# Optimization experiments

Measured on AMD Instinct MI355X. Metric: run time of the kernel, lower is better.

Reference implementation:

```python
import jax, jax.numpy as jnp
import numpy as np

N, E, B = 100000, 3200000, 512
D_IN, D_H, HID = 500, 64, 200
NUM_CLASSES = 80
EPS_BN = 1e-5


def _sage(x, src, dst, Wl, bl, Wr):
    # PyG SAGEConv (mean aggr): out = lin_l(mean_{j->i} x_j) + lin_r(x_i)
    n = x.shape[0]
    agg = jax.ops.segment_sum(x[src], dst, num_segments=n)          # [n, d_in]
    deg = jax.ops.segment_sum(jnp.ones((src.shape[0],), x.dtype), dst, num_segments=n)
    mean = agg / jnp.maximum(deg, 1.0)[:, None]
    return mean @ Wl + bl + x @ Wr


def _bn(c, g, b):
    # BatchNorm1d, training-mode batch statistics (biased var)
    mu = c.mean(0)
    var = c.var(0)
    return (c - mu) / jnp.sqrt(var + EPS_BN) * g + b


def setup_inputs() -> dict:
    key = jax.random.key(0)
    ks = jax.random.split(key, 16)
    p = lambda k, shape: jax.random.normal(k, shape, dtype=jnp.float32) * 0.05
    z = lambda d: jnp.zeros((d,), jnp.float32)
    o = lambda d: jnp.ones((d,), jnp.float32)
    return {
        "x": jax.random.uniform(ks[0], (N, D_IN), dtype=jnp.float32),
        "edge_index": jax.random.randint(ks[1], (2, E), 0, N),
        "batch": jnp.sort(jax.random.randint(ks[2], (N,), 0, B)),
        "y": jax.random.randint(ks[3], (B,), 0, NUM_CLASSES),
        "conv1_Wl": p(ks[4], (D_IN, D_H)), "conv1_bl": z(D_H), "conv1_Wr": p(ks[5], (D_IN, D_H)),
        "conv2_Wl": p(ks[6], (D_H, D_H)),  "conv2_bl": z(D_H), "conv2_Wr": p(ks[7], (D_H, D_H)),
        "conv3_Wl": p(ks[8], (D_H, D_H)),  "conv3_bl": z(D_H), "conv3_Wr": p(ks[9], (D_H, D_H)),
        "lin1_W": p(ks[10], (D_H, HID)), "lin1_b": z(HID),
        "bn1_g": o(HID), "bn1_beta": z(HID),
        "lin2_W": p(ks[11], (HID, HID // 2)), "lin2_b": z(HID // 2),
        "bn2_g": o(HID // 2), "bn2_beta": z(HID // 2),
        "lin3_W": p(ks[12], (HID // 2, HID // 2)), "lin3_b": z(HID // 2),
        "bn3_g": o(HID // 2), "bn3_beta": z(HID // 2),
        "lin4_W": p(ks[13], (HID // 2, NUM_CLASSES)), "lin4_b": z(NUM_CLASSES),
    }


def reference(x, edge_index, batch, y,
              conv1_Wl, conv1_bl, conv1_Wr,
              conv2_Wl, conv2_bl, conv2_Wr,
              conv3_Wl, conv3_bl, conv3_Wr,
              lin1_W, lin1_b, bn1_g, bn1_beta,
              lin2_W, lin2_b, bn2_g, bn2_beta,
              lin3_W, lin3_b, bn3_g, bn3_beta,
              lin4_W, lin4_b):
    src, dst = edge_index[0], edge_index[1]
    # F.normalize(x, p=1.0, dim=-1)
    xn = x / jnp.maximum(jnp.abs(x).sum(-1, keepdims=True), 1e-12)
    e = _sage(xn, src, dst, conv1_Wl, conv1_bl, conv1_Wr)
    e = _sage(e, src, dst, conv2_Wl, conv2_bl, conv2_Wr)
    e = _sage(e, src, dst, conv3_Wl, conv3_bl, conv3_Wr)
    # global_mean_pool over graph ids
    sums = jax.ops.segment_sum(e, batch, num_segments=B)             # [B, 64]
    cnts = jax.ops.segment_sum(jnp.ones((e.shape[0],), e.dtype), batch, num_segments=B)
    c = sums / jnp.maximum(cnts, 1.0)[:, None]
    # dropout (p=0.1) omitted for a deterministic reference
    c = c @ lin1_W + lin1_b
    b = jnp.tanh(_bn(c, bn1_g, bn1_beta))
    c = b @ lin2_W + lin2_b
    b = jnp.tanh(_bn(c, bn2_g, bn2_beta))
    c = b @ lin3_W + lin3_b
    b = jnp.tanh(_bn(c, bn3_g, bn3_beta))
    return b @ lin4_W + lin4_b                                       # [B, 80]
```

## Files before the change

### kernel.cpp

```cpp
#include <hip/hip_runtime.h>
#include <hip/hip_bf16.h>

#define NN 100000
#define NE 3200000
#define NB 512
#define DIN 500
#define DH 64
#define HIDN 200
#define NCLS 80

#define NBUK 256
#define NPB 391
#define EPB 16384
#define NBLK_E ((NE + EPB - 1) / EPB)

typedef __attribute__((ext_vector_type(8))) short bf16x8;
typedef __attribute__((ext_vector_type(4))) float f32x4;

__device__ __forceinline__ short f2bf(float f) {
    union { float f; unsigned u; } v; v.f = f;
    unsigned r = v.u + 0x7FFF + ((v.u >> 16) & 1);
    return (short)(r >> 16);
}
__device__ __forceinline__ float bf2f(short s) {
    union { unsigned u; float f; } v; v.u = ((unsigned)(unsigned short)s) << 16;
    return v.f;
}

__global__ void bukhist_kernel(const int* __restrict__ dst, int* __restrict__ block_hist) {
    __shared__ int h[NBUK];
    for (int i = threadIdx.x; i < NBUK; i += 256) h[i] = 0;
    __syncthreads();
    int base = blockIdx.x * EPB;
    int end = min(base + EPB, NE);
    for (int e = base + threadIdx.x; e < end; e += 256)
        atomicAdd(&h[dst[e] / NPB], 1);
    __syncthreads();
    for (int i = threadIdx.x; i < NBUK; i += 256)
        block_hist[blockIdx.x * NBUK + i] = h[i];
}

__global__ void bukoff_kernel(int* __restrict__ block_hist, int* __restrict__ buk_base) {
    __shared__ int tot[NBUK];
    __shared__ int sc[NBUK];
    int b = threadIdx.x;
    int s = 0;
    for (int i = 0; i < NBLK_E; ++i) s += block_hist[i * NBUK + b];
    tot[b] = s; sc[b] = s;
    __syncthreads();
    for (int o = 1; o < NBUK; o <<= 1) {
        int t = (b >= o) ? sc[b - o] : 0;
        __syncthreads();
        sc[b] += t;
        __syncthreads();
    }
    int excl = sc[b] - tot[b];
    buk_base[b] = excl;
    if (b == NBUK - 1) buk_base[NBUK] = excl + tot[b];
    int run = excl;
    for (int i = 0; i < NBLK_E; ++i) {
        int idx = i * NBUK + b;
        int v = block_hist[idx];
        block_hist[idx] = run;
        run += v;
    }
}

__global__ void bukscat_kernel(const int* __restrict__ src, const int* __restrict__ dst,
                               const int* __restrict__ block_hist, int* __restrict__ bpack) {
    __shared__ int cur[NBUK];
    for (int i = threadIdx.x; i < NBUK; i += 256)
        cur[i] = block_hist[blockIdx.x * NBUK + i];
    __syncthreads();
    int base = blockIdx.x * EPB;
    int end = min(base + EPB, NE);
    for (int e = base + threadIdx.x; e < end; e += 256) {
        int d = dst[e];
        int bk = d / NPB;
        int p = atomicAdd(&cur[bk], 1);
        bpack[p] = (src[e] << 9) | (d - bk * NPB);
    }
}

__global__ void bukfin_kernel(const int* __restrict__ buk_base, const int* __restrict__ bpack,
                              int* __restrict__ row_ptr, float* __restrict__ invdeg,
                              int* __restrict__ csr_src) {
    __shared__ int cnt[NPB];
    __shared__ int cbase[NPB];
    int bk = blockIdx.x;
    int n0 = bk * NPB;
    int nloc = min(n0 + NPB, NN) - n0;
    for (int i = threadIdx.x; i < nloc; i += 256) cnt[i] = 0;
    __syncthreads();
    int beg = buk_base[bk], end = buk_base[bk + 1];
    for (int p = beg + threadIdx.x; p < end; p += 256)
        atomicAdd(&cnt[bpack[p] & 511], 1);
    __syncthreads();
    if (threadIdx.x == 0) {
        int run = beg;
        for (int i = 0; i < nloc; ++i) { int v = cnt[i]; cbase[i] = run; run += v; }
    }
    __syncthreads();
    for (int i = threadIdx.x; i < nloc; i += 256) {
        row_ptr[n0 + i] = cbase[i];
        invdeg[n0 + i] = 1.0f / fmaxf((float)cnt[i], 1.0f);
        cnt[i] = cbase[i];
    }
    if (bk == NBUK - 1 && threadIdx.x == 0) row_ptr[NN] = end;
    __syncthreads();
    for (int p = beg + threadIdx.x; p < end; p += 256) {
        int v = bpack[p];
        int q = atomicAdd(&cnt[v & 511], 1);
        csr_src[q] = v >> 9;
    }
}

__global__ void wprep_kernel(const float* __restrict__ Wl, const float* __restrict__ Wr,
                             short* __restrict__ Wb, int K, int KP) {
    int id = blockIdx.x * blockDim.x + threadIdx.x;
    if (id >= 128 * KP) return;
    int col = id / KP, k = id - col * KP;
    float v = 0.f;
    if (k < K) v = (col < 64) ? Wl[(size_t)k * 64 + col] : Wr[(size_t)k * 64 + (col - 64)];
    Wb[(size_t)col * KP + k] = f2bf(v);
}

template<int KP, int KREAL, bool SCALE>
__launch_bounds__(256)
__global__ void gemm_mfma_pipe(const float* __restrict__ in, const short* __restrict__ Wb,
                               short* __restrict__ Hl, short* __restrict__ Hr) {
    __shared__ short A_lds[2][64][40];
    __shared__ short B_lds[2][128][40];
    __shared__ float s_red[64][4];
    const int tid = threadIdx.x;
    const int row0 = blockIdx.x * 64;
    const int w = tid >> 6, l = tid & 63;
    const int q = l >> 4, r16 = l & 15;
    const int sa_row = tid >> 2;
    const int sa_kc  = (tid & 3) * 8;
    const int ga_row = row0 + sa_row;
    const bool row_ok = ga_row < NN;
    const float* arow = in + (size_t)ga_row * KREAL;
    const int sb_col = tid >> 1;
    const int sb_kh  = (tid & 1) * 16;
    const short* bsrc = Wb + (size_t)sb_col * KP + sb_kh;

    f32x4 acc[8];
#pragma unroll
    for (int c = 0; c < 8; ++c) acc[c] = (f32x4){0.f, 0.f, 0.f, 0.f};
    float pabs = 0.f;
    float va[8];
    bf16x8 vb0, vb1;
    constexpr int NT = KP / 32;

    auto loadA = [&](int t) {
        int gk = t * 32 + sa_kc;
#pragma unroll
        for (int i = 0; i < 8; i += 4) {
            if (row_ok && (KP == KREAL || gk + i + 3 < KREAL)) {
                const float4 f = *(const float4*)(arow + gk + i);
                va[i] = f.x; va[i + 1] = f.y; va[i + 2] = f.z; va[i + 3] = f.w;
            } else {
#pragma unroll
                for (int j = 0; j < 4; ++j)
                    va[i + j] = (row_ok && gk + i + j < KREAL) ? arow[gk + i + j] : 0.f;
            }
        }
    };
    auto loadB = [&](int t) {
        vb0 = *(const bf16x8*)(bsrc + t * 32);
        vb1 = *(const bf16x8*)(bsrc + t * 32 + 8);
    };
    auto store = [&](int buf) {
        short s[8];
#pragma unroll
        for (int i = 0; i < 8; ++i) {
            if (SCALE) pabs += fabsf(va[i]);
            s[i] = f2bf(va[i]);
        }
        *(bf16x8*)&A_lds[buf][sa_row][sa_kc] = *(bf16x8*)s;
        *(bf16x8*)&B_lds[buf][sb_col][sb_kh] = vb0;
        *(bf16x8*)&B_lds[buf][sb_col][sb_kh + 8] = vb1;
    };

    loadA(0); loadB(0);
    store(0);
    __syncthreads();
    int cur = 0;
    for (int t = 0; t < NT; ++t) {
        if (t + 1 < NT) { loadA(t + 1); loadB(t + 1); }
        bf16x8 a = *(bf16x8*)&A_lds[cur][w * 16 + r16][q * 8];
#pragma unroll
        for (int c = 0; c < 8; ++c) {
            bf16x8 b = *(bf16x8*)&B_lds[cur][c * 16 + r16][q * 8];
            acc[c] = __builtin_amdgcn_mfma_f32_16x16x32_bf16(a, b, acc[c], 0, 0, 0);
        }
        if (t + 1 < NT) {
            store(cur ^ 1);
            __syncthreads();
            cur ^= 1;
        }
    }

    if (SCALE) {
        __syncthreads();
        s_red[sa_row][tid & 3] = pabs;
        __syncthreads();
        if (tid < 64) {
            float ss = s_red[tid][0] + s_red[tid][1] + s_red[tid][2] + s_red[tid][3];
            s_red[tid][0] = 1.0f / fmaxf(ss, 1e-12f);
        }
        __syncthreads();
    }

#pragma unroll
    for (int c = 0; c < 8; ++c) {
#pragma unroll
        for (int rr = 0; rr < 4; ++rr) {
            int lrow = w * 16 + q * 4 + rr;
            int grow = row0 + lrow;
            if (grow < NN) {
                float o = acc[c][rr];
                if (SCALE) o *= s_red[lrow][0];
                short ob = f2bf(o);
                if (c < 4) Hl[(size_t)grow * 64 + c * 16 + r16] = ob;
                else       Hr[(size_t)grow * 64 + (c - 4) * 16 + r16] = ob;
            }
        }
    }
}

__launch_bounds__(256)
__global__ void gemm64_mfma(const short* __restrict__ ein, const short* __restrict__ Wb,
                            short* __restrict__ Hl, short* __restrict__ Hr) {
    const int tid = threadIdx.x;
    const int row0 = blockIdx.x * 64;
    const int w = tid >> 6, l = tid & 63;
    const int q = l >> 4, r16 = l & 15;
    const int arow = row0 + w * 16 + r16;
    const bool ok = arow < NN;
    const short* ap = ein + (size_t)(ok ? arow : 0) * 64 + q * 8;
    f32x4 acc[8];
#pragma unroll
    for (int c = 0; c < 8; ++c) acc[c] = (f32x4){0.f, 0.f, 0.f, 0.f};
    const bf16x8 z8 = (bf16x8){0, 0, 0, 0, 0, 0, 0, 0};
#pragma unroll
    for (int t = 0; t < 2; ++t) {
        bf16x8 a = ok ? *(const bf16x8*)(ap + t * 32) : z8;
#pragma unroll
        for (int c = 0; c < 8; ++c) {
            bf16x8 b = *(const bf16x8*)(Wb + (size_t)(c * 16 + r16) * 64 + t * 32 + q * 8);
            acc[c] = __builtin_amdgcn_mfma_f32_16x16x32_bf16(a, b, acc[c], 0, 0, 0);
        }
    }
#pragma unroll
    for (int c = 0; c < 8; ++c) {
#pragma unroll
        for (int rr = 0; rr < 4; ++rr) {
            int grow = row0 + w * 16 + q * 4 + rr;
            if (grow < NN) {
                short ob = f2bf(acc[c][rr]);
                if (c < 4) Hl[(size_t)grow * 64 + c * 16 + r16] = ob;
                else       Hr[(size_t)grow * 64 + (c - 4) * 16 + r16] = ob;
            }
        }
    }
}

__launch_bounds__(256)
__global__ void gather_kernel(const int* __restrict__ row_ptr, const int* __restrict__ csr_src,
                              const short* __restrict__ Hl, const short* __restrict__ Hr,
                              const float* __restrict__ invdeg, const float* __restrict__ bl,
                              short* __restrict__ eout) {
    int node = blockIdx.x * 4 + (threadIdx.x >> 6);
    if (node >= NN) return;
    int lane = threadIdx.x & 63;
    int ng = lane >> 3;
    int fl = lane & 7;
    int beg = row_ptr[node], end = row_ptr[node + 1];
    float a0[8], a1[8];
#pragma unroll
    for (int j = 0; j < 8; ++j) { a0[j] = 0.f; a1[j] = 0.f; }
    int p = beg + ng;
    for (; p + 8 < end; p += 16) {
        int s0 = csr_src[p];
        int s1 = csr_src[p + 8];
        bf16x8 v0 = *(const bf16x8*)(Hl + (size_t)s0 * 64 + fl * 8);
        bf16x8 v1 = *(const bf16x8*)(Hl + (size_t)s1 * 64 + fl * 8);
#pragma unroll
        for (int j = 0; j < 8; ++j) { a0[j] += bf2f(v0[j]); a1[j] += bf2f(v1[j]); }
    }
    if (p < end) {
        int s0 = csr_src[p];
        bf16x8 v0 = *(const bf16x8*)(Hl + (size_t)s0 * 64 + fl * 8);
#pragma unroll
        for (int j = 0; j < 8; ++j) a0[j] += bf2f(v0[j]);
    }
#pragma unroll
    for (int j = 0; j < 8; ++j) a0[j] += a1[j];
#pragma unroll
    for (int m = 8; m < 64; m <<= 1)
#pragma unroll
        for (int j = 0; j < 8; ++j) a0[j] += __shfl_xor(a0[j], m, 64);
    if (ng == 0) {
        float idg = invdeg[node];
        bf16x8 hr = *(const bf16x8*)(Hr + (size_t)node * 64 + fl * 8);
        short o[8];
#pragma unroll
        for (int j = 0; j < 8; ++j)
            o[j] = f2bf(a0[j] * idg + bl[fl * 8 + j] + bf2f(hr[j]));
        *(bf16x8*)(eout + (size_t)node * 64 + fl * 8) = *(bf16x8*)o;
    }
}

__global__ void gseg_kernel(const int* __restrict__ batch, int* __restrict__ gstart) {
    int i = blockIdx.x * blockDim.x + threadIdx.x;
    if (i >= NN) return;
    int bc = batch[i];
    int bp = (i == 0) ? -1 : batch[i - 1];
    for (int b = bp + 1; b <= bc; ++b) gstart[b] = i;
    if (i == NN - 1)
        for (int b = bc + 1; b <= NB; ++b) gstart[b] = NN;
}

__launch_bounds__(256)
__global__ void pool_seg(const short* __restrict__ e, const int* __restrict__ gstart,
                         float* __restrict__ c0) {
    __shared__ float part[4][64];
    int b = blockIdx.x;
    int w = threadIdx.x >> 6, lane = threadIdx.x & 63;
    int s = gstart[b], t = gstart[b + 1];
    float acc = 0.f;
    for (int i = s + w; i < t; i += 4) acc += bf2f(e[(size_t)i * 64 + lane]);
    part[w][lane] = acc;
    __syncthreads();
    if (w == 0) {
        float v = part[0][lane] + part[1][lane] + part[2][lane] + part[3][lane];
        c0[b * 64 + lane] = v / fmaxf((float)(t - s), 1.0f);
    }
}

__global__ void lin_kernel(const float* __restrict__ in, const float* __restrict__ W,
                           const float* __restrict__ bias, float* __restrict__ out,
                           int Kd, int Dout) {
    int id = blockIdx.x * blockDim.x + threadIdx.x;
    if (id >= NB * Dout) return;
    int row = id / Dout, col = id - row * Dout;
    const float* ir = in + (size_t)row * Kd;
    float acc = bias[col];
    for (int k = 0; k < Kd; ++k) acc += ir[k] * W[(size_t)k * Dout + col];
    out[id] = acc;
}

__global__ void bnstats_kernel(const float* __restrict__ c, const float* __restrict__ g,
                               const float* __restrict__ beta, float* __restrict__ sa,
                               float* __restrict__ sb, int Dout) {
    int col = blockIdx.x;
    int tid = threadIdx.x;
    float s = 0.f, sq = 0.f;
    for (int r = tid; r < NB; r += 256) {
        float v = c[(size_t)r * Dout + col];
        s += v; sq += v * v;
    }
    __shared__ float ls[256], lq[256];
    ls[tid] = s; lq[tid] = sq;
    __syncthreads();
    for (int o = 128; o > 0; o >>= 1) {
        if (tid < o) { ls[tid] += ls[tid + o]; lq[tid] += lq[tid + o]; }
        __syncthreads();
    }
    if (tid == 0) {
        float mu = ls[0] / NB;
        float var = lq[0] / NB - mu * mu;
        float a = g[col] * rsqrtf(var + 1e-5f);
        sa[col] = a;
        sb[col] = beta[col] - mu * a;
    }
}

__global__ void bnapply_kernel(const float* __restrict__ c, const float* __restrict__ sa,
                               const float* __restrict__ sb, float* __restrict__ bv, int Dout) {
    int id = blockIdx.x * blockDim.x + threadIdx.x;
    if (id >= NB * Dout) return;
    int col = id % Dout;
    bv[id] = tanhf(c[id] * sa[col] + sb[col]);
}

extern "C" void kernel_launch(void* const* d_in, const int* in_sizes, int n_in,
                              void* d_out, int out_size, void* d_ws, size_t ws_size,
                              hipStream_t stream) {
    const float* x    = (const float*)d_in[0];
    const int* ei     = (const int*)d_in[1];
    const int* src    = ei;
    const int* dst    = ei + NE;
    const int* batch  = (const int*)d_in[2];
    const float* c1Wl = (const float*)d_in[4];
    const float* c1bl = (const float*)d_in[5];
    const float* c1Wr = (const float*)d_in[6];
    const float* c2Wl = (const float*)d_in[7];
    const float* c2bl = (const float*)d_in[8];
    const float* c2Wr = (const float*)d_in[9];
    const float* c3Wl = (const float*)d_in[10];
    const float* c3bl = (const float*)d_in[11];
    const float* c3Wr = (const float*)d_in[12];
    const float* l1W  = (const float*)d_in[13]; const float* l1b = (const float*)d_in[14];
    const float* bn1g = (const float*)d_in[15]; const float* bn1b = (const float*)d_in[16];
    const float* l2W  = (const float*)d_in[17]; const float* l2b = (const float*)d_in[18];
    const float* bn2g = (const float*)d_in[19]; const float* bn2b = (const float*)d_in[20];
    const float* l3W  = (const float*)d_in[21]; const float* l3b = (const float*)d_in[22];
    const float* bn3g = (const float*)d_in[23]; const float* bn3b = (const float*)d_in[24];
    const float* l4W  = (const float*)d_in[25]; const float* l4b = (const float*)d_in[26];
    float* out = (float*)d_out;

    char* wsb = (char*)d_ws;
    short* Hl     = (short*)wsb; wsb += (size_t)NN * 64 * 2;
    short* Hr     = (short*)wsb; wsb += (size_t)NN * 64 * 2;
    short* e      = (short*)wsb; wsb += (size_t)NN * 64 * 2;
    float* invdeg = (float*)wsb; wsb += (size_t)NN * 4;
    float* c      = (float*)wsb; wsb += (size_t)NB * HIDN * 4;
    float* bv     = (float*)wsb; wsb += (size_t)NB * HIDN * 4;
    float* sa     = (float*)wsb; wsb += HIDN * 4;
    float* sb     = (float*)wsb; wsb += HIDN * 4;
    short* Wb1    = (short*)wsb; wsb += 128 * 512 * 2;
    short* Wb2    = (short*)wsb; wsb += 128 * 64 * 2;
    short* Wb3    = (short*)wsb; wsb += 128 * 64 * 2;
    int* row_ptr  = (int*)wsb;   wsb += (size_t)(NN + 1) * 4;
    int* csr_src  = (int*)wsb;   wsb += (size_t)NE * 4;
    int* buk_base = (int*)wsb;   wsb += (NBUK + 1) * 4;
    int* gstart   = (int*)wsb;   wsb += (NB + 1) * 4;
    int* bpack      = (int*)Hl;
    int* block_hist = (int*)e;

    bukhist_kernel<<<NBLK_E, 256, 0, stream>>>(dst, block_hist);
    bukoff_kernel<<<1, NBUK, 0, stream>>>(block_hist, buk_base);
    bukscat_kernel<<<NBLK_E, 256, 0, stream>>>(src, dst, block_hist, bpack);
    bukfin_kernel<<<NBUK, 256, 0, stream>>>(buk_base, bpack, row_ptr, invdeg, csr_src);

    gseg_kernel<<<(NN + 255) / 256, 256, 0, stream>>>(batch, gstart);

    wprep_kernel<<<(128 * 512 + 255) / 256, 256, 0, stream>>>(c1Wl, c1Wr, Wb1, DIN, 512);
    wprep_kernel<<<(128 * 64 + 255) / 256, 256, 0, stream>>>(c2Wl, c2Wr, Wb2, DH, 64);
    wprep_kernel<<<(128 * 64 + 255) / 256, 256, 0, stream>>>(c3Wl, c3Wr, Wb3, DH, 64);

    const int GB = (NN + 63) / 64;
    const int GGB = (NN + 3) / 4;

    gemm_mfma_pipe<512, DIN, true><<<GB, 256, 0, stream>>>(x, Wb1, Hl, Hr);
    gather_kernel<<<GGB, 256, 0, stream>>>(row_ptr, csr_src, Hl, Hr, invdeg, c1bl, e);
    gemm64_mfma<<<GB, 256, 0, stream>>>(e, Wb2, Hl, Hr);
    gather_kernel<<<GGB, 256, 0, stream>>>(row_ptr, csr_src, Hl, Hr, invdeg, c2bl, e);
    gemm64_mfma<<<GB, 256, 0, stream>>>(e, Wb3, Hl, Hr);
    gather_kernel<<<GGB, 256, 0, stream>>>(row_ptr, csr_src, Hl, Hr, invdeg, c3bl, e);

    pool_seg<<<NB, 256, 0, stream>>>(e, gstart, bv);

    lin_kernel<<<(NB * 200 + 255) / 256, 256, 0, stream>>>(bv, l1W, l1b, c, 64, 200);
    bnstats_kernel<<<200, 256, 0, stream>>>(c, bn1g, bn1b, sa, sb, 200);
    bnapply_kernel<<<(NB * 200 + 255) / 256, 256, 0, stream>>>(c, sa, sb, bv, 200);

    lin_kernel<<<(NB * 100 + 255) / 256, 256, 0, stream>>>(bv, l2W, l2b, c, 200, 100);
    bnstats_kernel<<<100, 256, 0, stream>>>(c, bn2g, bn2b, sa, sb, 100);
    bnapply_kernel<<<(NB * 100 + 255) / 256, 256, 0, stream>>>(c, sa, sb, bv, 100);

    lin_kernel<<<(NB * 100 + 255) / 256, 256, 0, stream>>>(bv, l3W, l3b, c, 100, 100);
    bnstats_kernel<<<100, 256, 0, stream>>>(c, bn3g, bn3b, sa, sb, 100);
    bnapply_kernel<<<(NB * 100 + 255) / 256, 256, 0, stream>>>(c, sa, sb, bv, 100);

    lin_kernel<<<(NB * 80 + 255) / 256, 256, 0, stream>>>(bv, l4W, l4b, out, 100, 80);
}
```

Before: 575.8 us.

## Enlarge first GEMM tile, keep Hr and final embeddings in fp32, deepen gather unroll

The first SAGE GEMM now processes 128 rows per block, with each wave computing two 16-row fragments that share the B loads, and uses a two-stage register prefetch over the 500-wide input. The root-term Hr and the last layer's output are now stored in fp32 instead of bf16, which adds memory traffic but improves accuracy. The gather loop is unrolled to four outstanding neighbour loads per lane, and its launch bounds request 8 blocks per CU. Together these aim to cut per-tile overhead in the large GEMM and to hide gather latency, at the cost of more registers and more bytes moved for Hr.

Result: slower. 608.4 us (+5.7%).

```diff
diff --git a/kernel.cpp b/kernel.cpp
--- a/kernel.cpp
+++ b/kernel.cpp
@@ -125,114 +125,112 @@
     Wb[(size_t)col * KP + k] = f2bf(v);
 }
 
-template<int KP, int KREAL, bool SCALE>
 __launch_bounds__(256)
 __global__ void gemm_mfma_pipe(const float* __restrict__ in, const short* __restrict__ Wb,
-                               short* __restrict__ Hl, short* __restrict__ Hr) {
-    __shared__ short A_lds[2][64][40];
+                               short* __restrict__ Hl, float* __restrict__ Hr) {
+    __shared__ short A_lds[2][128][40];
     __shared__ short B_lds[2][128][40];
-    __shared__ float s_red[64][4];
+    __shared__ float s_red[128][2];
     const int tid = threadIdx.x;
-    const int row0 = blockIdx.x * 64;
+    const int row0 = blockIdx.x * 128;
     const int w = tid >> 6, l = tid & 63;
     const int q = l >> 4, r16 = l & 15;
-    const int sa_row = tid >> 2;
-    const int sa_kc  = (tid & 3) * 8;
+    const int sa_row = tid >> 1;
+    const int sa_kc  = (tid & 1) * 16;
     const int ga_row = row0 + sa_row;
     const bool row_ok = ga_row < NN;
-    const float* arow = in + (size_t)ga_row * KREAL;
-    const int sb_col = tid >> 1;
-    const int sb_kh  = (tid & 1) * 16;
-    const short* bsrc = Wb + (size_t)sb_col * KP + sb_kh;
-
-    f32x4 acc[8];
-#pragma unroll
-    for (int c = 0; c < 8; ++c) acc[c] = (f32x4){0.f, 0.f, 0.f, 0.f};
+    const float* arow = in + (size_t)ga_row * DIN + sa_kc;
+    const short* bsrc = Wb + (size_t)sa_row * 512 + sa_kc;
+
+    f32x4 acc0[8], acc1[8];
+#pragma unroll
+    for (int c = 0; c < 8; ++c) { acc0[c] = (f32x4){0.f,0.f,0.f,0.f}; acc1[c] = (f32x4){0.f,0.f,0.f,0.f}; }
     float pabs = 0.f;
-    float va[8];
-    bf16x8 vb0, vb1;
-    constexpr int NT = KP / 32;
-
-    auto loadA = [&](int t) {
-        int gk = t * 32 + sa_kc;
-#pragma unroll
-        for (int i = 0; i < 8; i += 4) {
-            if (row_ok && (KP == KREAL || gk + i + 3 < KREAL)) {
-                const float4 f = *(const float4*)(arow + gk + i);
-                va[i] = f.x; va[i + 1] = f.y; va[i + 2] = f.z; va[i + 3] = f.w;
-            } else {
-#pragma unroll
-                for (int j = 0; j < 4; ++j)
-                    va[i + j] = (row_ok && gk + i + j < KREAL) ? arow[gk + i + j] : 0.f;
-            }
-        }
-    };
-    auto loadB = [&](int t) {
-        vb0 = *(const bf16x8*)(bsrc + t * 32);
-        vb1 = *(const bf16x8*)(bsrc + t * 32 + 8);
-    };
-    auto store = [&](int buf) {
-        short s[8];
-#pragma unroll
-        for (int i = 0; i < 8; ++i) {
-            if (SCALE) pabs += fabsf(va[i]);
-            s[i] = f2bf(va[i]);
-        }
-        *(bf16x8*)&A_lds[buf][sa_row][sa_kc] = *(bf16x8*)s;
-        *(bf16x8*)&B_lds[buf][sb_col][sb_kh] = vb0;
-        *(bf16x8*)&B_lds[buf][sb_col][sb_kh + 8] = vb1;
-    };
-
-    loadA(0); loadB(0);
-    store(0);
-    __syncthreads();
-    int cur = 0;
-    for (int t = 0; t < NT; ++t) {
-        if (t + 1 < NT) { loadA(t + 1); loadB(t + 1); }
-        bf16x8 a = *(bf16x8*)&A_lds[cur][w * 16 + r16][q * 8];
-#pragma unroll
-        for (int c = 0; c < 8; ++c) {
-            bf16x8 b = *(bf16x8*)&B_lds[cur][c * 16 + r16][q * 8];
-            acc[c] = __builtin_amdgcn_mfma_f32_16x16x32_bf16(a, b, acc[c], 0, 0, 0);
-        }
-        if (t + 1 < NT) {
-            store(cur ^ 1);
-            __syncthreads();
-            cur ^= 1;
-        }
-    }
-
-    if (SCALE) {
+    float va0[16], va1[16];
+    bf16x8 vb00, vb01, vb10, vb11;
+
+#define ISSUE(T, S) do { \
+    _Pragma("unroll") \
+    for (int i = 0; i < 16; i += 4) { \
+        int gk = (T) * 32 + sa_kc + i; \
+        float4 f = (row_ok && gk < DIN) ? *(const float4*)(arow + (T) * 32 + i) \
+                                        : make_float4(0.f, 0.f, 0.f, 0.f); \
+        va##S[i] = f.x; va##S[i+1] = f.y; va##S[i+2] = f.z; va##S[i+3] = f.w; \
+    } \
+    vb##S##0 = *(const bf16x8*)(bsrc + (T) * 32); \
+    vb##S##1 = *(const bf16x8*)(bsrc + (T) * 32 + 8); \
+} while (0)
+
+#define STAGE(BUF, S) do { \
+    short sh[16]; \
+    _Pragma("unroll") \
+    for (int i = 0; i < 16; ++i) { pabs += fabsf(va##S[i]); sh[i] = f2bf(va##S[i]); } \
+    *(bf16x8*)&A_lds[BUF][sa_row][sa_kc]     = *(bf16x8*)&sh[0]; \
+    *(bf16x8*)&A_lds[BUF][sa_row][sa_kc + 8] = *(bf16x8*)&sh[8]; \
+    *(bf16x8*)&B_lds[BUF][sa_row][sa_kc]     = vb##S##0; \
+    *(bf16x8*)&B_lds[BUF][sa_row][sa_kc + 8] = vb##S##1; \
+} while (0)
+
+#define COMPUTE(BUF) do { \
+    bf16x8 a0 = *(bf16x8*)&A_lds[BUF][w * 32 + r16][q * 8]; \
+    bf16x8 a1 = *(bf16x8*)&A_lds[BUF][w * 32 + 16 + r16][q * 8]; \
+    _Pragma("unroll") \
+    for (int c = 0; c < 8; ++c) { \
+        bf16x8 b = *(bf16x8*)&B_lds[BUF][c * 16 + r16][q * 8]; \
+        acc0[c] = __builtin_amdgcn_mfma_f32_16x16x32_bf16(a0, b, acc0[c], 0, 0, 0); \
+        acc1[c] = __builtin_amdgcn_mfma_f32_16x16x32_bf16(a1, b, acc1[c], 0, 0, 0); \
+    } \
+} while (0)
+
+    ISSUE(0, 0); ISSUE(1, 1);
+    STAGE(0, 0);
+    __syncthreads();
+    for (int tt = 0; tt < 8; ++tt) {
+        int t0 = tt * 2;
+        if (tt < 7) ISSUE(t0 + 2, 0);
+        COMPUTE(0);
+        STAGE(1, 1);
         __syncthreads();
-        s_red[sa_row][tid & 3] = pabs;
-        __syncthreads();
-        if (tid < 64) {
-            float ss = s_red[tid][0] + s_red[tid][1] + s_red[tid][2] + s_red[tid][3];
-            s_red[tid][0] = 1.0f / fmaxf(ss, 1e-12f);
-        }
-        __syncthreads();
-    }
-
-#pragma unroll
-    for (int c = 0; c < 8; ++c) {
-#pragma unroll
-        for (int rr = 0; rr < 4; ++rr) {
-            int lrow = w * 16 + q * 4 + rr;
-            int grow = row0 + lrow;
-            if (grow < NN) {
-                float o = acc[c][rr];
-                if (SCALE) o *= s_red[lrow][0];
-                short ob = f2bf(o);
-                if (c < 4) Hl[(size_t)grow * 64 + c * 16 + r16] = ob;
-                else       Hr[(size_t)grow * 64 + (c - 4) * 16 + r16] = ob;
-            }
-        }
-    }
+        if (tt < 7) ISSUE(t0 + 3, 1);
+        COMPUTE(1);
+        if (tt < 7) { STAGE(0, 0); __syncthreads(); }
+    }
+#undef ISSUE
+#undef STAGE
+#undef COMPUTE
+
+    __syncthreads();
+    s_red[sa_row][tid & 1] = pabs;
+    __syncthreads();
+    if (tid < 128) {
+        float ss = s_red[tid][0] + s_red[tid][1];
+        s_red[tid][0] = 1.0f / fmaxf(ss, 1e-12f);
+    }
+    __syncthreads();
+
+#define EPI(RF, ACC) do { \
+    _Pragma("unroll") \
+    for (int c = 0; c < 8; ++c) { \
+        _Pragma("unroll") \
+        for (int rr = 0; rr < 4; ++rr) { \
+            int lrow = w * 32 + (RF) * 16 + q * 4 + rr; \
+            int grow = row0 + lrow; \
+            if (grow < NN) { \
+                float o = ACC[c][rr] * s_red[lrow][0]; \
+                if (c < 4) Hl[(size_t)grow * 64 + c * 16 + r16] = f2bf(o); \
+                else       Hr[(size_t)grow * 64 + (c - 4) * 16 + r16] = o; \
+            } \
+        } \
+    } \
+} while (0)
+    EPI(0, acc0);
+    EPI(1, acc1);
+#undef EPI
 }
 
 __launch_bounds__(256)
 __global__ void gemm64_mfma(const short* __restrict__ ein, const short* __restrict__ Wb,
-                            short* __restrict__ Hl, short* __restrict__ Hr) {
+                            short* __restrict__ Hl, float* __restrict__ Hr) {
     const int tid = threadIdx.x;
     const int row0 = blockIdx.x * 64;
     const int w = tid >> 6, l = tid & 63;
@@ -259,19 +257,19 @@
         for (int rr = 0; rr < 4; ++rr) {
             int grow = row0 + w * 16 + q * 4 + rr;
             if (grow < NN) {
-                short ob = f2bf(acc[c][rr]);
-                if (c < 4) Hl[(size_t)grow * 64 + c * 16 + r16] = ob;
-                else       Hr[(size_t)grow * 64 + (c - 4) * 16 + r16] = ob;
+                if (c < 4) Hl[(size_t)grow * 64 + c * 16 + r16] = f2bf(acc[c][rr]);
+                else       Hr[(size_t)grow * 64 + (c - 4) * 16 + r16] = acc[c][rr];
             }
         }
     }
 }
 
-__launch_bounds__(256)
+template<bool LAST>
+__launch_bounds__(256, 8)
 __global__ void gather_kernel(const int* __restrict__ row_ptr, const int* __restrict__ csr_src,
-                              const short* __restrict__ Hl, const short* __restrict__ Hr,
+                              const short* __restrict__ Hl, const float* __restrict__ Hr,
                               const float* __restrict__ invdeg, const float* __restrict__ bl,
-                              short* __restrict__ eout) {
+                              short* __restrict__ ebf, float* __restrict__ ef32) {
     int node = blockIdx.x * 4 + (threadIdx.x >> 6);
     if (node >= NN) return;
     int lane = threadIdx.x & 63;
@@ -282,15 +280,22 @@
 #pragma unroll
     for (int j = 0; j < 8; ++j) { a0[j] = 0.f; a1[j] = 0.f; }
     int p = beg + ng;
-    for (; p + 8 < end; p += 16) {
+    for (; p + 24 < end; p += 32) {
         int s0 = csr_src[p];
         int s1 = csr_src[p + 8];
+        int s2 = csr_src[p + 16];
+        int s3 = csr_src[p + 24];
         bf16x8 v0 = *(const bf16x8*)(Hl + (size_t)s0 * 64 + fl * 8);
         bf16x8 v1 = *(const bf16x8*)(Hl + (size_t)s1 * 64 + fl * 8);
-#pragma unroll
-        for (int j = 0; j < 8; ++j) { a0[j] += bf2f(v0[j]); a1[j] += bf2f(v1[j]); }
-    }
-    if (p < end) {
+        bf16x8 v2 = *(const bf16x8*)(Hl + (size_t)s2 * 64 + fl * 8);
+        bf16x8 v3 = *(const bf16x8*)(Hl + (size_t)s3 * 64 + fl * 8);
+#pragma unroll
+        for (int j = 0; j < 8; ++j) {
+            a0[j] += bf2f(v0[j]) + bf2f(v2[j]);
+            a1[j] += bf2f(v1[j]) + bf2f(v3[j]);
+        }
+    }
+    for (; p < end; p += 8) {
         int s0 = csr_src[p];
         bf16x8 v0 = *(const bf16x8*)(Hl + (size_t)s0 * 64 + fl * 8);
 #pragma unroll
@@ -304,12 +309,26 @@
         for (int j = 0; j < 8; ++j) a0[j] += __shfl_xor(a0[j], m, 64);
     if (ng == 0) {
         float idg = invdeg[node];
-        bf16x8 hr = *(const bf16x8*)(Hr + (size_t)node * 64 + fl * 8);
-        short o[8];
-#pragma unroll
-        for (int j = 0; j < 8; ++j)
-            o[j] = f2bf(a0[j] * idg + bl[fl * 8 + j] + bf2f(hr[j]));
-        *(bf16x8*)(eout + (size_t)node * 64 + fl * 8) = *(bf16x8*)o;
+        const float4 h0 = *(const float4*)(Hr + (size_t)node * 64 + fl * 8);
+        const float4 h1 = *(const float4*)(Hr + (size_t)node * 64 + fl * 8 + 4);
+        float o[8];
+        o[0] = a0[0] * idg + bl[fl * 8 + 0] + h0.x;
+        o[1] = a0[1] * idg + bl[fl * 8 + 1] + h0.y;
+        o[2] = a0[2] * idg + bl[fl * 8 + 2] + h0.z;
+        o[3] = a0[3] * idg + bl[fl * 8 + 3] + h0.w;
+        o[4] = a0[4] * idg + bl[fl * 8 + 4] + h1.x;
+        o[5] = a0[5] * idg + bl[fl * 8 + 5] + h1.y;
+        o[6] = a0[6] * idg + bl[fl * 8 + 6] + h1.z;
+        o[7] = a0[7] * idg + bl[fl * 8 + 7] + h1.w;
+        if (LAST) {
+            *(float4*)(ef32 + (size_t)node * 64 + fl * 8)     = make_float4(o[0], o[1], o[2], o[3]);
+            *(float4*)(ef32 + (size_t)node * 64 + fl * 8 + 4) = make_float4(o[4], o[5], o[6], o[7]);
+        } else {
+            short s[8];
+#pragma unroll
+            for (int j = 0; j < 8; ++j) s[j] = f2bf(o[j]);
+            *(bf16x8*)(ebf + (size_t)node * 64 + fl * 8) = *(bf16x8*)s;
+        }
     }
 }
 
@@ -324,14 +343,14 @@
 }
 
 __launch_bounds__(256)
-__global__ void pool_seg(const short* __restrict__ e, const int* __restrict__ gstart,
+__global__ void pool_seg(const float* __restrict__ e, const int* __restrict__ gstart,
                          float* __restrict__ c0) {
     __shared__ float part[4][64];
     int b = blockIdx.x;
     int w = threadIdx.x >> 6, lane = threadIdx.x & 63;
     int s = gstart[b], t = gstart[b + 1];
     float acc = 0.f;
-    for (int i = s + w; i < t; i += 4) acc += bf2f(e[(size_t)i * 64 + lane]);
+    for (int i = s + w; i < t; i += 4) acc += e[(size_t)i * 64 + lane];
     part[w][lane] = acc;
     __syncthreads();
     if (w == 0) {
@@ -414,8 +433,9 @@
 
     char* wsb = (char*)d_ws;
     short* Hl     = (short*)wsb; wsb += (size_t)NN * 64 * 2;
-    short* Hr     = (short*)wsb; wsb += (size_t)NN * 64 * 2;
+    float* Hr     = (float*)wsb; wsb += (size_t)NN * 64 * 4;
     short* e      = (short*)wsb; wsb += (size_t)NN * 64 * 2;
+    float* e3     = (float*)wsb; wsb += (size_t)NN * 64 * 4;
     float* invdeg = (float*)wsb; wsb += (size_t)NN * 4;
     float* c      = (float*)wsb; wsb += (size_t)NB * HIDN * 4;
     float* bv     = (float*)wsb; wsb += (size_t)NB * HIDN * 4;
@@ -442,17 +462,18 @@
     wprep_kernel<<<(128 * 64 + 255) / 256, 256, 0, stream>>>(c2Wl, c2Wr, Wb2, DH, 64);
     wprep_kernel<<<(128 * 64 + 255) / 256, 256, 0, stream>>>(c3Wl, c3Wr, Wb3, DH, 64);
 
-    const int GB = (NN + 63) / 64;
-    const int GGB = (NN + 3) / 4;
-
-    gemm_mfma_pipe<512, DIN, true><<<GB, 256, 0, stream>>>(x, Wb1, Hl, Hr);
-    gather_kernel<<<GGB, 256, 0, stream>>>(row_ptr, csr_src, Hl, Hr, invdeg, c1bl, e);
-    gemm64_mfma<<<GB, 256, 0, stream>>>(e, Wb2, Hl, Hr);
-    gather_kernel<<<GGB, 256, 0, stream>>>(row_ptr, csr_src, Hl, Hr, invdeg, c2bl, e);
-    gemm64_mfma<<<GB, 256, 0, stream>>>(e, Wb3, Hl, Hr);
-    gather_kernel<<<GGB, 256, 0, stream>>>(row_ptr, csr_src, Hl, Hr, invdeg, c3bl, e);
-
-    pool_seg<<<NB, 256, 0, stream>>>(e, gstart, bv);
+    const int GB128 = (NN + 127) / 128;
+    const int GB64  = (NN + 63) / 64;
+    const int GGB   = (NN + 3) / 4;
+
+    gemm_mfma_pipe<<<GB128, 256, 0, stream>>>(x, Wb1, Hl, Hr);
+    gather_kernel<false><<<GGB, 256, 0, stream>>>(row_ptr, csr_src, Hl, Hr, invdeg, c1bl, e, e3);
+    gemm64_mfma<<<GB64, 256, 0, stream>>>(e, Wb2, Hl, Hr);
+    gather_kernel<false><<<GGB, 256, 0, stream>>>(row_ptr, csr_src, Hl, Hr, invdeg, c2bl, e, e3);
+    gemm64_mfma<<<GB64, 256, 0, stream>>>(e, Wb3, Hl, Hr);
+    gather_kernel<true><<<GGB, 256, 0, stream>>>(row_ptr, csr_src, Hl, Hr, invdeg, c3bl, e, e3);
+
+    pool_seg<<<NB, 256, 0, stream>>>(e3, gstart, bv);
 
     lin_kernel<<<(NB * 200 + 255) / 256, 256, 0, stream>>>(bv, l1W, l1b, c, 64, 200);
     bnstats_kernel<<<200, 256, 0, stream>>>(c, bn1g, bn1b, sa, sb, 200);
```
